# Performance work log

Hardware: AMD Instinct MI355X
Metric: run time of the kernel (lower is better)

## Reference

```python
import jax, jax.numpy as jnp
import numpy as np

N_QUBITS = 8
BATCH = 65536
# conv pairs [control, target]; pooling is CRY(pi/4) with control=sink(=pair[1]), target=source(=pair[0])
_PAIRS = ((0, 1), (2, 3), (4, 5), (6, 7), (0, 2), (4, 6), (0, 4))
_PI4 = jnp.asarray(np.pi / 4, dtype=jnp.float32)


def _crz(phi):
    # diag(1,1,e^{-i phi/2}, e^{+i phi/2}) -- PennyLane CRZ convention
    U = jnp.eye(4, dtype=jnp.complex64)
    return U.at[2, 2].set(jnp.exp(-0.5j * phi)).at[3, 3].set(jnp.exp(0.5j * phi))


def _crx(phi):
    c = jnp.cos(phi / 2).astype(jnp.complex64)
    s = jnp.sin(phi / 2).astype(jnp.complex64)
    U = jnp.eye(4, dtype=jnp.complex64)
    return U.at[2, 2].set(c).at[3, 3].set(c).at[2, 3].set(-1j * s).at[3, 2].set(-1j * s)


def _cry(phi):
    c = jnp.cos(phi / 2).astype(jnp.complex64)
    s = jnp.sin(phi / 2).astype(jnp.complex64)
    U = jnp.eye(4, dtype=jnp.complex64)
    return U.at[2, 2].set(c).at[3, 3].set(c).at[2, 3].set(-s).at[3, 2].set(s)


def _apply2(psi, U, c, t):
    # psi: (B, 2,...,2) rank 1+N_QUBITS; apply 4x4 U on qubits (c, t)
    psi = jnp.moveaxis(psi, (c + 1, t + 1), (N_QUBITS - 1, N_QUBITS))
    sh = psi.shape
    psi = psi.reshape(sh[:-2] + (4,)) @ U.T
    psi = psi.reshape(sh)
    return jnp.moveaxis(psi, (N_QUBITS - 1, N_QUBITS), (c + 1, t + 1))


def _qcnn(x, weights):
    half = x.astype(jnp.float32) / 2  # (B, 8)
    # RX(theta)|0> = [cos(theta/2), -i sin(theta/2)]; initial state is a product state
    f = jnp.stack([jnp.cos(half).astype(jnp.complex64), (-1j * jnp.sin(half)).astype(jnp.complex64)], axis=-1)  # (B,8,2)
    psi = f[:, 0, :]
    for q in range(1, N_QUBITS):
        psi = jnp.einsum('b...,bq->b...q', psi, f[:, q, :])  # (B,2,...,2)
    # deferred-measurement form of mid-circuit measure + cond(RY(pi/4)):
    for k, (a, b) in enumerate(_PAIRS):
        psi = _apply2(psi, _crz(weights[k, 0]), a, b)
        psi = _apply2(psi, _crx(weights[k, 1]), a, b)
        psi = _apply2(psi, _cry(_PI4), b, a)
    probs0 = jnp.sum(jnp.abs(psi) ** 2, axis=tuple(range(2, N_QUBITS + 1)))  # (B, 2) marginal of wire 0
    return (probs0[:, 0] - probs0[:, 1]).astype(jnp.float32)  # <Z_0>


def setup_inputs() -> dict:
    key = jax.random.key(0)
    k1, k2 = jax.random.split(key)
    x = jax.random.normal(k1, (BATCH, N_QUBITS), dtype=jnp.float32)
    weights = jax.random.normal(k2, (7, 2), dtype=jnp.float32)
    return {"x": x, "weights": weights}


def reference(x, weights):
    return _qcnn(x, weights)
```

## Files before the change

kernel.cpp:

```cpp
#include <hip/hip_runtime.h>
#include <math.h>

#define NPAIRS 7

__device__ __forceinline__ float2 cmul(float2 a, float2 b) {
    return make_float2(fmaf(a.x, b.x, -a.y * b.y), fmaf(a.x, b.y, a.y * b.x));
}
__device__ __forceinline__ float2 cmulc(float2 a, float2 b) {
    return make_float2(fmaf(a.x, b.x, a.y * b.y), fmaf(a.y, b.x, -a.x * b.y));
}
__device__ __forceinline__ float2 cadd(float2 a, float2 b) {
    return make_float2(a.x + b.x, a.y + b.y);
}

struct Herm { float d0, d1; float2 o; };

__device__ __forceinline__ Herm chan(const Herm A, const Herm B, const float2* __restrict__ Mk) {
    float2 Mr[16];
#pragma unroll
    for (int i = 0; i < 16; ++i) Mr[i] = Mk[i];

    float2 Af[2][2], Bf[2][2];
    Af[0][0] = make_float2(A.d0, 0.f);       Af[0][1] = A.o;
    Af[1][0] = make_float2(A.o.x, -A.o.y);   Af[1][1] = make_float2(A.d1, 0.f);
    Bf[0][0] = make_float2(B.d0, 0.f);       Bf[0][1] = B.o;
    Bf[1][0] = make_float2(B.o.x, -B.o.y);   Bf[1][1] = make_float2(B.d1, 0.f);

    float2 rho[4][4];
#pragma unroll
    for (int i = 0; i < 2; ++i)
#pragma unroll
        for (int m = 0; m < 2; ++m)
#pragma unroll
            for (int k = 0; k < 2; ++k)
#pragma unroll
                for (int l = 0; l < 2; ++l)
                    rho[2 * i + m][2 * k + l] = cmul(Af[i][k], Bf[m][l]);

    float2 N[4][4];
#pragma unroll
    for (int p = 0; p < 4; ++p)
#pragma unroll
        for (int s = 0; s < 4; ++s) {
            float2 acc = make_float2(0.f, 0.f);
#pragma unroll
            for (int r = 0; r < 4; ++r) acc = cadd(acc, cmul(Mr[4 * p + r], rho[r][s]));
            N[p][s] = acc;
        }

#define TPQ(p, q)                                                        \
    ({                                                                   \
        float2 acc_ = make_float2(0.f, 0.f);                             \
        _Pragma("unroll")                                                \
        for (int s_ = 0; s_ < 4; ++s_)                                   \
            acc_ = cadd(acc_, cmulc(N[p][s_], Mr[4 * (q) + s_]));        \
        acc_;                                                            \
    })

    float2 t00 = TPQ(0, 0);
    float2 t11 = TPQ(1, 1);
    float2 t22 = TPQ(2, 2);
    float2 t33 = TPQ(3, 3);
    float2 t02 = TPQ(0, 2);
    float2 t13 = TPQ(1, 3);
#undef TPQ

    Herm R;
    R.d0 = t00.x + t11.x;
    R.d1 = t22.x + t33.x;
    R.o  = cadd(t02, t13);
    return R;
}

extern "C" __global__ void __launch_bounds__(256)
qcnn_kernel(const float* __restrict__ x, const float* __restrict__ w,
            float* __restrict__ out, int batch)
{
    __shared__ float2 M[NPAIRS][16];

    const int tid = threadIdx.x;
    if (tid < NPAIRS) {
        const int k = tid;
        const float w0 = w[2 * k];
        const float w1 = w[2 * k + 1];
        float zr, zi, c1, s1;
        sincosf(0.5f * w0, &zi, &zr);
        sincosf(0.5f * w1, &s1, &c1);
        const float cy = 0.92387953251128674f;
        const float sy = 0.38268343236508978f;

#pragma unroll
        for (int i = 0; i < 16; ++i) M[k][i] = make_float2(0.f, 0.f);

        M[k][4 * 0 + 0] = make_float2(1.f, 0.f);
        M[k][4 * 1 + 1] = make_float2(cy, 0.f);
        M[k][4 * 1 + 2] = make_float2(sy * s1 * zi, sy * s1 * zr);
        M[k][4 * 1 + 3] = make_float2(-sy * c1 * zr, -sy * c1 * zi);
        M[k][4 * 2 + 2] = make_float2(c1 * zr, -c1 * zi);
        M[k][4 * 2 + 3] = make_float2(s1 * zi, -s1 * zr);
        M[k][4 * 3 + 1] = make_float2(sy, 0.f);
        M[k][4 * 3 + 2] = make_float2(-cy * s1 * zi, -cy * s1 * zr);
        M[k][4 * 3 + 3] = make_float2(cy * c1 * zr, cy * c1 * zi);
    }
    __syncthreads();

    const int idx = blockIdx.x * 256 + tid;
    if (idx >= batch) return;

    const float4 xa = reinterpret_cast<const float4*>(x)[2 * idx];
    const float4 xb = reinterpret_cast<const float4*>(x)[2 * idx + 1];
    const float xv[8] = {xa.x, xa.y, xa.z, xa.w, xb.x, xb.y, xb.z, xb.w};

    Herm r[8];
#pragma unroll
    for (int q = 0; q < 8; ++q) {
        float s, c;
        sincosf(xv[q], &s, &c);
        r[q].d0 = 0.5f * (1.f + c);
        r[q].d1 = 0.5f * (1.f - c);
        r[q].o  = make_float2(0.f, 0.5f * s);
    }

    const Herm r01 = chan(r[0], r[1], M[0]);
    const Herm r23 = chan(r[2], r[3], M[1]);
    const Herm r45 = chan(r[4], r[5], M[2]);
    const Herm r67 = chan(r[6], r[7], M[3]);
    const Herm rA  = chan(r01, r23, M[4]);
    const Herm rB  = chan(r45, r67, M[5]);
    const Herm rF  = chan(rA, rB, M[6]);

    out[idx] = rF.d0 - rF.d1;
}

extern "C" void kernel_launch(void* const* d_in, const int* in_sizes, int n_in,
                              void* d_out, int out_size, void* d_ws, size_t ws_size,
                              hipStream_t stream) {
    const float* x = (const float*)d_in[0];
    const float* w = (const float*)d_in[1];
    float* out = (float*)d_out;
    const int batch = in_sizes[0] / 8;
    const int block = 256;
    const int grid = (batch + block - 1) / block;
    qcnn_kernel<<<grid, block, 0, stream>>>(x, w, out, batch);
}
```

Baseline: 12.01 us.

## Precompute real-valued 2-qubit channel coefficients in setup kernel, shrink per-thread math

Each two-qubit channel is folded into a real 3x16 coefficient matrix that acts on the outer product of the two inputs' (trace-normalized) Bloch-like parameters. A separate single-block setup kernel computes these coefficients into workspace, and the main kernel then does 48 FMAs per channel instead of full complex 4x4 density-matrix conjugation. This cuts per-element ALU work a lot, but adds a second kernel launch and a dependency on workspace memory, with coefficients read from global memory instead of LDS.

```diff
diff --git a/kernel.cpp b/kernel.cpp
--- a/kernel.cpp
+++ b/kernel.cpp
@@ -13,70 +13,18 @@
     return make_float2(a.x + b.x, a.y + b.y);
 }
 
-struct Herm { float d0, d1; float2 o; };
-
-__device__ __forceinline__ Herm chan(const Herm A, const Herm B, const float2* __restrict__ Mk) {
-    float2 Mr[16];
-#pragma unroll
-    for (int i = 0; i < 16; ++i) Mr[i] = Mk[i];
-
-    float2 Af[2][2], Bf[2][2];
-    Af[0][0] = make_float2(A.d0, 0.f);       Af[0][1] = A.o;
-    Af[1][0] = make_float2(A.o.x, -A.o.y);   Af[1][1] = make_float2(A.d1, 0.f);
-    Bf[0][0] = make_float2(B.d0, 0.f);       Bf[0][1] = B.o;
-    Bf[1][0] = make_float2(B.o.x, -B.o.y);   Bf[1][1] = make_float2(B.d1, 0.f);
-
-    float2 rho[4][4];
-#pragma unroll
-    for (int i = 0; i < 2; ++i)
-#pragma unroll
-        for (int m = 0; m < 2; ++m)
-#pragma unroll
-            for (int k = 0; k < 2; ++k)
-#pragma unroll
-                for (int l = 0; l < 2; ++l)
-                    rho[2 * i + m][2 * k + l] = cmul(Af[i][k], Bf[m][l]);
-
-    float2 N[4][4];
-#pragma unroll
-    for (int p = 0; p < 4; ++p)
-#pragma unroll
-        for (int s = 0; s < 4; ++s) {
-            float2 acc = make_float2(0.f, 0.f);
-#pragma unroll
-            for (int r = 0; r < 4; ++r) acc = cadd(acc, cmul(Mr[4 * p + r], rho[r][s]));
-            N[p][s] = acc;
-        }
-
-#define TPQ(p, q)                                                        \
-    ({                                                                   \
-        float2 acc_ = make_float2(0.f, 0.f);                             \
-        _Pragma("unroll")                                                \
-        for (int s_ = 0; s_ < 4; ++s_)                                   \
-            acc_ = cadd(acc_, cmulc(N[p][s_], Mr[4 * (q) + s_]));        \
-        acc_;                                                            \
-    })
-
-    float2 t00 = TPQ(0, 0);
-    float2 t11 = TPQ(1, 1);
-    float2 t22 = TPQ(2, 2);
-    float2 t33 = TPQ(3, 3);
-    float2 t02 = TPQ(0, 2);
-    float2 t13 = TPQ(1, 3);
-#undef TPQ
-
-    Herm R;
-    R.d0 = t00.x + t11.x;
-    R.d1 = t22.x + t33.x;
-    R.o  = cadd(t02, t13);
-    return R;
+__device__ __forceinline__ float2 alphav(int i, int k, int e) {
+    if (i == 0 && k == 0) return make_float2(e == 1 ? 1.f : 0.f, 0.f);
+    if (i == 0 && k == 1) return make_float2(e == 2 ? 1.f : 0.f, e == 3 ? 1.f : 0.f);
+    if (i == 1 && k == 0) return make_float2(e == 2 ? 1.f : 0.f, e == 3 ? -1.f : 0.f);
+    return make_float2(e == 0 ? 1.f : (e == 1 ? -1.f : 0.f), 0.f);
 }
 
-extern "C" __global__ void __launch_bounds__(256)
-qcnn_kernel(const float* __restrict__ x, const float* __restrict__ w,
-            float* __restrict__ out, int batch)
+__global__ void __launch_bounds__(512)
+qcnn_setup(const float* __restrict__ w, float* __restrict__ cw)
 {
-    __shared__ float2 M[NPAIRS][16];
+    __shared__ float2 Msh[NPAIRS][16];
+    __shared__ float2 Ksh[NPAIRS][2][16];
 
     const int tid = threadIdx.x;
     if (tid < NPAIRS) {
@@ -90,46 +38,115 @@
         const float sy = 0.38268343236508978f;
 
 #pragma unroll
-        for (int i = 0; i < 16; ++i) M[k][i] = make_float2(0.f, 0.f);
+        for (int i = 0; i < 16; ++i) Msh[k][i] = make_float2(0.f, 0.f);
 
-        M[k][4 * 0 + 0] = make_float2(1.f, 0.f);
-        M[k][4 * 1 + 1] = make_float2(cy, 0.f);
-        M[k][4 * 1 + 2] = make_float2(sy * s1 * zi, sy * s1 * zr);
-        M[k][4 * 1 + 3] = make_float2(-sy * c1 * zr, -sy * c1 * zi);
-        M[k][4 * 2 + 2] = make_float2(c1 * zr, -c1 * zi);
-        M[k][4 * 2 + 3] = make_float2(s1 * zi, -s1 * zr);
-        M[k][4 * 3 + 1] = make_float2(sy, 0.f);
-        M[k][4 * 3 + 2] = make_float2(-cy * s1 * zi, -cy * s1 * zr);
-        M[k][4 * 3 + 3] = make_float2(cy * c1 * zr, cy * c1 * zi);
+        Msh[k][4 * 0 + 0] = make_float2(1.f, 0.f);
+        Msh[k][4 * 1 + 1] = make_float2(cy, 0.f);
+        Msh[k][4 * 1 + 2] = make_float2(sy * s1 * zi, sy * s1 * zr);
+        Msh[k][4 * 1 + 3] = make_float2(-sy * c1 * zr, -sy * c1 * zi);
+        Msh[k][4 * 2 + 2] = make_float2(c1 * zr, -c1 * zi);
+        Msh[k][4 * 2 + 3] = make_float2(s1 * zi, -s1 * zr);
+        Msh[k][4 * 3 + 1] = make_float2(sy, 0.f);
+        Msh[k][4 * 3 + 2] = make_float2(-cy * s1 * zi, -cy * s1 * zr);
+        Msh[k][4 * 3 + 3] = make_float2(cy * c1 * zr, cy * c1 * zi);
     }
     __syncthreads();
 
-    const int idx = blockIdx.x * 256 + tid;
+    if (tid < NPAIRS * 32) {
+        const int p = tid >> 5;
+        const int which = (tid >> 4) & 1;
+        const int e = tid & 15;
+        const int r = e >> 2, s = e & 3;
+        float2 res;
+        if (which == 0)
+            res = cadd(cmulc(Msh[p][0 * 4 + r], Msh[p][0 * 4 + s]),
+                       cmulc(Msh[p][1 * 4 + r], Msh[p][1 * 4 + s]));
+        else
+            res = cadd(cmulc(Msh[p][0 * 4 + r], Msh[p][2 * 4 + s]),
+                       cmulc(Msh[p][1 * 4 + r], Msh[p][3 * 4 + s]));
+        Ksh[p][which][e] = res;
+    }
+    __syncthreads();
+
+    if (tid < NPAIRS * 48) {
+        const int p = tid / 48;
+        const int rem = tid % 48;
+        const int outm = rem >> 4;
+        const int ef = rem & 15;
+        const int e = ef >> 2, f = ef & 3;
+        const float2* K = Ksh[p][outm == 0 ? 0 : 1];
+        float2 acc = make_float2(0.f, 0.f);
+        for (int r = 0; r < 4; ++r)
+            for (int s = 0; s < 4; ++s) {
+                const int i = r >> 1, m = r & 1, k = s >> 1, l = s & 1;
+                const float2 a = alphav(i, k, e);
+                const float2 b = alphav(m, l, f);
+                acc = cadd(acc, cmul(cmul(K[r * 4 + s], a), b));
+            }
+        cw[tid] = (outm == 2) ? acc.y : acc.x;
+    }
+}
+
+struct H3 { float d0, re, im; };
+
+__device__ __forceinline__ void outer16(const H3 A, const H3 B, float wv[16]) {
+    const float u1 = A.d0, u2 = A.re, u3 = A.im;
+    const float v1 = B.d0, v2 = B.re, v3 = B.im;
+    wv[0] = 1.f;      wv[1] = v1;       wv[2] = v2;       wv[3] = v3;
+    wv[4] = u1;       wv[5] = u1 * v1;  wv[6] = u1 * v2;  wv[7] = u1 * v3;
+    wv[8] = u2;       wv[9] = u2 * v1;  wv[10] = u2 * v2; wv[11] = u2 * v3;
+    wv[12] = u3;      wv[13] = u3 * v1; wv[14] = u3 * v2; wv[15] = u3 * v3;
+}
+
+__device__ __forceinline__ H3 chan3(const H3 A, const H3 B, const float* __restrict__ c) {
+    float wv[16];
+    outer16(A, B, wv);
+    float d = 0.f, re = 0.f, im = 0.f;
+#pragma unroll
+    for (int t = 0; t < 16; ++t) {
+        d  = fmaf(c[t],      wv[t], d);
+        re = fmaf(c[16 + t], wv[t], re);
+        im = fmaf(c[32 + t], wv[t], im);
+    }
+    H3 R; R.d0 = d; R.re = re; R.im = im;
+    return R;
+}
+
+__global__ void __launch_bounds__(256)
+qcnn_main(const float* __restrict__ x, const float* __restrict__ cw,
+          float* __restrict__ out, int batch)
+{
+    const int idx = blockIdx.x * 256 + threadIdx.x;
     if (idx >= batch) return;
 
     const float4 xa = reinterpret_cast<const float4*>(x)[2 * idx];
     const float4 xb = reinterpret_cast<const float4*>(x)[2 * idx + 1];
     const float xv[8] = {xa.x, xa.y, xa.z, xa.w, xb.x, xb.y, xb.z, xb.w};
 
-    Herm r[8];
+    H3 r[8];
 #pragma unroll
     for (int q = 0; q < 8; ++q) {
         float s, c;
         sincosf(xv[q], &s, &c);
         r[q].d0 = 0.5f * (1.f + c);
-        r[q].d1 = 0.5f * (1.f - c);
-        r[q].o  = make_float2(0.f, 0.5f * s);
+        r[q].re = 0.f;
+        r[q].im = 0.5f * s;
     }
 
-    const Herm r01 = chan(r[0], r[1], M[0]);
-    const Herm r23 = chan(r[2], r[3], M[1]);
-    const Herm r45 = chan(r[4], r[5], M[2]);
-    const Herm r67 = chan(r[6], r[7], M[3]);
-    const Herm rA  = chan(r01, r23, M[4]);
-    const Herm rB  = chan(r45, r67, M[5]);
-    const Herm rF  = chan(rA, rB, M[6]);
+    const H3 r01 = chan3(r[0], r[1], cw + 0 * 48);
+    const H3 r23 = chan3(r[2], r[3], cw + 1 * 48);
+    const H3 r45 = chan3(r[4], r[5], cw + 2 * 48);
+    const H3 r67 = chan3(r[6], r[7], cw + 3 * 48);
+    const H3 rA  = chan3(r01, r23, cw + 4 * 48);
+    const H3 rB  = chan3(r45, r67, cw + 5 * 48);
 
-    out[idx] = rF.d0 - rF.d1;
+    float wv[16];
+    outer16(rA, rB, wv);
+    float d = 0.f;
+#pragma unroll
+    for (int t = 0; t < 16; ++t) d = fmaf(cw[6 * 48 + t], wv[t], d);
+
+    out[idx] = 2.f * d - 1.f;
 }
 
 extern "C" void kernel_launch(void* const* d_in, const int* in_sizes, int n_in,
@@ -138,8 +155,9 @@
     const float* x = (const float*)d_in[0];
     const float* w = (const float*)d_in[1];
     float* out = (float*)d_out;
+    float* cw = (float*)d_ws;
     const int batch = in_sizes[0] / 8;
-    const int block = 256;
-    const int grid = (batch + block - 1) / block;
-    qcnn_kernel<<<grid, block, 0, stream>>>(x, w, out, batch);
+
+    qcnn_setup<<<1, 512, 0, stream>>>(w, cw);
+    qcnn_main<<<(batch + 255) / 256, 256, 0, stream>>>(x, cw, out, batch);
 }
```

After: 14.82 us. 1.23x slower.

## Specialize 2-qubit channel algebra and compute channel coefficients per thread

Applied to the files above, without the earlier changes.

Replaces the generic 4x4 complex conjugation M·rho·M† with a closed-form expansion that uses the sparsity of M and trace normalization. Each density matrix is now stored as d0 plus one complex off-diagonal, and the final stage computes only the diagonal. Shared-memory channel setup and the block barrier are removed; every thread recomputes the channel coefficients from the weights using fast __sincosf intrinsics. This trades a large drop in FLOPs for redundant per-thread weight math and lower-precision trig.

```diff
diff --git a/kernel.cpp b/kernel.cpp
--- a/kernel.cpp
+++ b/kernel.cpp
@@ -1,7 +1,5 @@
 #include <hip/hip_runtime.h>
 #include <math.h>
-
-#define NPAIRS 7
 
 __device__ __forceinline__ float2 cmul(float2 a, float2 b) {
     return make_float2(fmaf(a.x, b.x, -a.y * b.y), fmaf(a.x, b.y, a.y * b.x));
@@ -12,124 +10,143 @@
 __device__ __forceinline__ float2 cadd(float2 a, float2 b) {
     return make_float2(a.x + b.x, a.y + b.y);
 }
+__device__ __forceinline__ float2 cscale(float s, float2 a) {
+    return make_float2(s * a.x, s * a.y);
+}
+__device__ __forceinline__ float2 conjf2(float2 a) { return make_float2(a.x, -a.y); }
 
-struct Herm { float d0, d1; float2 o; };
+struct H3 { float d0; float2 o; };
 
-__device__ __forceinline__ Herm chan(const Herm A, const Herm B, const float2* __restrict__ Mk) {
-    float2 Mr[16];
-#pragma unroll
-    for (int i = 0; i < 16; ++i) Mr[i] = Mk[i];
+struct Chan {
+    float k11, k22, k33;
+    float2 k12, k13, k23;
+    float2 c22, c23;
+    float ko11;
+    float2 ko12, ko13, ko21, ko22, ko23, ko31, ko32, ko33;
+};
 
-    float2 Af[2][2], Bf[2][2];
-    Af[0][0] = make_float2(A.d0, 0.f);       Af[0][1] = A.o;
-    Af[1][0] = make_float2(A.o.x, -A.o.y);   Af[1][1] = make_float2(A.d1, 0.f);
-    Bf[0][0] = make_float2(B.d0, 0.f);       Bf[0][1] = B.o;
-    Bf[1][0] = make_float2(B.o.x, -B.o.y);   Bf[1][1] = make_float2(B.d1, 0.f);
+__device__ __forceinline__ Chan mkchan(float w0, float w1) {
+    const float cy = 0.92387953251128674f;
+    const float sy = 0.38268343236508978f;
+    float zr, zi, c1, s1;
+    __sincosf(0.5f * w0, &zi, &zr);
+    __sincosf(0.5f * w1, &s1, &c1);
+    const float2 m12 = make_float2( sy * s1 * zi,  sy * s1 * zr);
+    const float2 m13 = make_float2(-sy * c1 * zr, -sy * c1 * zi);
+    const float2 m22 = make_float2( c1 * zr,      -c1 * zi);
+    const float2 m23 = make_float2( s1 * zi,      -s1 * zr);
+    const float2 m32 = make_float2(-cy * s1 * zi, -cy * s1 * zr);
+    const float2 m33 = make_float2( cy * c1 * zr,  cy * c1 * zi);
+    Chan C;
+    C.k11 = cy * cy;
+    C.k12 = cscale(cy, conjf2(m12));
+    C.k13 = cscale(cy, conjf2(m13));
+    C.k22 = fmaf(m12.x, m12.x, m12.y * m12.y);
+    C.k23 = cmulc(m12, m13);
+    C.k33 = fmaf(m13.x, m13.x, m13.y * m13.y);
+    C.c22 = conjf2(m22);
+    C.c23 = conjf2(m23);
+    C.ko11 = cy * sy;
+    C.ko12 = cscale(cy, conjf2(m32));
+    C.ko13 = cscale(cy, conjf2(m33));
+    C.ko21 = cscale(sy, m12);
+    C.ko22 = cmulc(m12, m32);
+    C.ko23 = cmulc(m12, m33);
+    C.ko31 = cscale(sy, m13);
+    C.ko32 = cmulc(m13, m32);
+    C.ko33 = cmulc(m13, m33);
+    return C;
+}
 
-    float2 rho[4][4];
-#pragma unroll
-    for (int i = 0; i < 2; ++i)
-#pragma unroll
-        for (int m = 0; m < 2; ++m)
-#pragma unroll
-            for (int k = 0; k < 2; ++k)
-#pragma unroll
-                for (int l = 0; l < 2; ++l)
-                    rho[2 * i + m][2 * k + l] = cmul(Af[i][k], Bf[m][l]);
+__device__ __forceinline__ float chanD(const H3 A, const H3 B, const Chan& C) {
+    const float a0 = A.d0, b0 = B.d0;
+    const float p = a0 * b0;
+    const float r11 = a0 - p, r22 = b0 - p, r33 = 1.f - a0 - b0 + p;
+    const float2 rho12 = cmulc(A.o, B.o);
+    const float2 rho13 = cscale(1.f - b0, A.o);
+    const float2 rho23 = cscale(1.f - a0, B.o);
+    float t = C.k12.x * rho12.x - C.k12.y * rho12.y
+            + C.k13.x * rho13.x - C.k13.y * rho13.y
+            + C.k23.x * rho23.x - C.k23.y * rho23.y;
+    float d = p;
+    d = fmaf(C.k11, r11, d);
+    d = fmaf(C.k22, r22, d);
+    d = fmaf(C.k33, r33, d);
+    return fmaf(2.f, t, d);
+}
 
-    float2 N[4][4];
-#pragma unroll
-    for (int p = 0; p < 4; ++p)
-#pragma unroll
-        for (int s = 0; s < 4; ++s) {
-            float2 acc = make_float2(0.f, 0.f);
-#pragma unroll
-            for (int r = 0; r < 4; ++r) acc = cadd(acc, cmul(Mr[4 * p + r], rho[r][s]));
-            N[p][s] = acc;
-        }
+__device__ __forceinline__ H3 chanK(const H3 A, const H3 B, const Chan& C) {
+    const float a0 = A.d0, b0 = B.d0;
+    const float p = a0 * b0;
+    const float r11 = a0 - p, r22 = b0 - p, r33 = 1.f - a0 - b0 + p;
+    const float2 rho12 = cmulc(A.o, B.o);
+    const float2 rho13 = cscale(1.f - b0, A.o);
+    const float2 rho23 = cscale(1.f - a0, B.o);
+    const float2 rho02 = cscale(b0, A.o);
+    const float2 rho03 = cmul(A.o, B.o);
 
-#define TPQ(p, q)                                                        \
-    ({                                                                   \
-        float2 acc_ = make_float2(0.f, 0.f);                             \
-        _Pragma("unroll")                                                \
-        for (int s_ = 0; s_ < 4; ++s_)                                   \
-            acc_ = cadd(acc_, cmulc(N[p][s_], Mr[4 * (q) + s_]));        \
-        acc_;                                                            \
-    })
-
-    float2 t00 = TPQ(0, 0);
-    float2 t11 = TPQ(1, 1);
-    float2 t22 = TPQ(2, 2);
-    float2 t33 = TPQ(3, 3);
-    float2 t02 = TPQ(0, 2);
-    float2 t13 = TPQ(1, 3);
-#undef TPQ
-
-    Herm R;
-    R.d0 = t00.x + t11.x;
-    R.d1 = t22.x + t33.x;
-    R.o  = cadd(t02, t13);
+    H3 R;
+    {
+        float t = C.k12.x * rho12.x - C.k12.y * rho12.y
+                + C.k13.x * rho13.x - C.k13.y * rho13.y
+                + C.k23.x * rho23.x - C.k23.y * rho23.y;
+        float d = p;
+        d = fmaf(C.k11, r11, d);
+        d = fmaf(C.k22, r22, d);
+        d = fmaf(C.k33, r33, d);
+        R.d0 = fmaf(2.f, t, d);
+    }
+    float2 o = cmul(rho02, C.c22);
+    o = cadd(o, cmul(rho03, C.c23));
+    o.x = fmaf(C.ko11, r11, o.x);
+    o = cadd(o, cmul(C.ko12, rho12));
+    o = cadd(o, cmul(C.ko13, rho13));
+    o = cadd(o, cmulc(C.ko21, rho12));
+    o = cadd(o, cscale(r22, C.ko22));
+    o = cadd(o, cmul(C.ko23, rho23));
+    o = cadd(o, cmulc(C.ko31, rho13));
+    o = cadd(o, cmulc(C.ko32, rho23));
+    o = cadd(o, cscale(r33, C.ko33));
+    R.o = o;
     return R;
 }
 
-extern "C" __global__ void __launch_bounds__(256)
-qcnn_kernel(const float* __restrict__ x, const float* __restrict__ w,
-            float* __restrict__ out, int batch)
+__global__ void __launch_bounds__(256, 1)
+qcnn_fused(const float* __restrict__ x, const float* __restrict__ w,
+           float* __restrict__ out, int batch)
 {
-    __shared__ float2 M[NPAIRS][16];
-
-    const int tid = threadIdx.x;
-    if (tid < NPAIRS) {
-        const int k = tid;
-        const float w0 = w[2 * k];
-        const float w1 = w[2 * k + 1];
-        float zr, zi, c1, s1;
-        sincosf(0.5f * w0, &zi, &zr);
-        sincosf(0.5f * w1, &s1, &c1);
-        const float cy = 0.92387953251128674f;
-        const float sy = 0.38268343236508978f;
-
-#pragma unroll
-        for (int i = 0; i < 16; ++i) M[k][i] = make_float2(0.f, 0.f);
-
-        M[k][4 * 0 + 0] = make_float2(1.f, 0.f);
-        M[k][4 * 1 + 1] = make_float2(cy, 0.f);
-        M[k][4 * 1 + 2] = make_float2(sy * s1 * zi, sy * s1 * zr);
-        M[k][4 * 1 + 3] = make_float2(-sy * c1 * zr, -sy * c1 * zi);
-        M[k][4 * 2 + 2] = make_float2(c1 * zr, -c1 * zi);
-        M[k][4 * 2 + 3] = make_float2(s1 * zi, -s1 * zr);
-        M[k][4 * 3 + 1] = make_float2(sy, 0.f);
-        M[k][4 * 3 + 2] = make_float2(-cy * s1 * zi, -cy * s1 * zr);
-        M[k][4 * 3 + 3] = make_float2(cy * c1 * zr, cy * c1 * zi);
-    }
-    __syncthreads();
-
-    const int idx = blockIdx.x * 256 + tid;
+    const int idx = blockIdx.x * 256 + threadIdx.x;
     if (idx >= batch) return;
 
     const float4 xa = reinterpret_cast<const float4*>(x)[2 * idx];
     const float4 xb = reinterpret_cast<const float4*>(x)[2 * idx + 1];
     const float xv[8] = {xa.x, xa.y, xa.z, xa.w, xb.x, xb.y, xb.z, xb.w};
 
-    Herm r[8];
+    H3 r[8];
 #pragma unroll
     for (int q = 0; q < 8; ++q) {
         float s, c;
-        sincosf(xv[q], &s, &c);
+        __sincosf(xv[q], &s, &c);
         r[q].d0 = 0.5f * (1.f + c);
-        r[q].d1 = 0.5f * (1.f - c);
         r[q].o  = make_float2(0.f, 0.5f * s);
     }
 
-    const Herm r01 = chan(r[0], r[1], M[0]);
-    const Herm r23 = chan(r[2], r[3], M[1]);
-    const Herm r45 = chan(r[4], r[5], M[2]);
-    const Herm r67 = chan(r[6], r[7], M[3]);
-    const Herm rA  = chan(r01, r23, M[4]);
-    const Herm rB  = chan(r45, r67, M[5]);
-    const Herm rF  = chan(rA, rB, M[6]);
+    const Chan C0 = mkchan(w[0],  w[1]);
+    const H3 r01 = chanK(r[0], r[1], C0);
+    const Chan C1 = mkchan(w[2],  w[3]);
+    const H3 r23 = chanK(r[2], r[3], C1);
+    const Chan C2 = mkchan(w[4],  w[5]);
+    const H3 r45 = chanK(r[4], r[5], C2);
+    const Chan C3 = mkchan(w[6],  w[7]);
+    const H3 r67 = chanK(r[6], r[7], C3);
+    const Chan C4 = mkchan(w[8],  w[9]);
+    const H3 rA  = chanK(r01, r23, C4);
+    const Chan C5 = mkchan(w[10], w[11]);
+    const H3 rB  = chanK(r45, r67, C5);
+    const Chan C6 = mkchan(w[12], w[13]);
+    const float d = chanD(rA, rB, C6);
 
-    out[idx] = rF.d0 - rF.d1;
+    out[idx] = 2.f * d - 1.f;
 }
 
 extern "C" void kernel_launch(void* const* d_in, const int* in_sizes, int n_in,
@@ -139,7 +156,5 @@
     const float* w = (const float*)d_in[1];
     float* out = (float*)d_out;
     const int batch = in_sizes[0] / 8;
-    const int block = 256;
-    const int grid = (batch + block - 1) / block;
-    qcnn_kernel<<<grid, block, 0, stream>>>(x, w, out, batch);
+    qcnn_fused<<<(batch + 255) / 256, 256, 0, stream>>>(x, w, out, batch);
 }
```

Result: faster. 9.688 us (-19.3%).
